# Kernel tuning notes

Hardware: AMD Instinct MI355X
Metric: run time of the kernel (lower is better)

## Reference

```python
import jax, jax.numpy as jnp
import numpy as np

E = 2048      # embed_dim
H = 16        # num_heads
HD = E // H // 2   # differential head dim = 64
S = 2048      # seq len
B = 1         # batch
DEPTH = 12
LAMBDA_INIT = 0.8 - 0.6 * float(np.exp(-0.3 * DEPTH))
EPS = 1e-5


def setup_inputs() -> dict:
    key = jax.random.key(0)
    ks = jax.random.split(key, 12)
    n = lambda k, shape, s=1.0: (jax.random.normal(k, shape, dtype=jnp.float32) * s)
    return {
        "query": n(ks[0], (S, B, E)),
        "key": n(ks[1], (S, B, E)),
        "value": n(ks[2], (S, B, E)),
        "rel_pos": 0,
        "attn_mask": jnp.zeros((B, S), dtype=jnp.bool_),
        "Wq": n(ks[3], (E, E), 0.02),
        "Wk": n(ks[4], (E, E), 0.02),
        "Wv": n(ks[5], (E, E), 0.02),
        "Wo": n(ks[6], (E, E), 0.02),
        "lq1": n(ks[7], (HD,), 0.1),
        "lk1": n(ks[8], (HD,), 0.1),
        "lq2": n(ks[9], (HD,), 0.1),
        "lk2": n(ks[10], (HD,), 0.1),
        "subln_g": jnp.ones((2 * HD,), dtype=jnp.float32),
    }


def reference(query, key, value, rel_pos, attn_mask,
              Wq, Wk, Wv, Wo, lq1, lk1, lq2, lk2, subln_g):
    # (S,B,E) -> (B,S,E)
    q = jnp.einsum("sbe,fe->bsf", query, Wq)
    k = jnp.einsum("sbe,fe->bsf", key, Wk)
    v = jnp.einsum("sbe,fe->bsf", value, Wv)

    bsz, tgt_len, _ = q.shape
    scaling = HD ** -0.5

    q = q.reshape(bsz, tgt_len, 2 * H, HD).transpose(0, 2, 1, 3) * scaling  # (B,2H,S,hd)
    k = k.reshape(bsz, tgt_len, 2 * H, HD).transpose(0, 2, 1, 3)            # (B,2H,S,hd)
    v = v.reshape(bsz, tgt_len, H, 2 * HD).transpose(0, 2, 1, 3)            # (B,H,S,2hd)

    scores = jnp.einsum("bhqd,bhkd->bhqk", q, k)  # (B,2H,S,S)
    mask = jnp.where(attn_mask[:, None, None, :], -jnp.inf, 0.0).astype(scores.dtype)
    scores = jnp.nan_to_num(scores + mask)  # torch.nan_to_num: nan->0, -inf->finite min

    probs = jax.nn.softmax(scores.astype(jnp.float32), axis=-1).astype(scores.dtype)
    probs = jnp.clip(probs, -1e6, 1e6)  # clamp as in original (dropout is identity in eval)

    lam1 = jnp.exp(jnp.sum(lq1 * lk1))
    lam2 = jnp.exp(jnp.sum(lq2 * lk2))
    lam_full = lam1 - lam2 + LAMBDA_INIT

    probs = probs.reshape(bsz, H, 2, tgt_len, tgt_len)
    diff = probs[:, :, 0] - lam_full * probs[:, :, 1]   # (B,H,S,S)

    attn = jnp.einsum("bhqk,bhkd->bhqd", diff, v)       # (B,H,S,2hd)

    # RMSNorm over last dim with affine weight
    rms = jax.lax.rsqrt(jnp.mean(jnp.square(attn), axis=-1, keepdims=True) + EPS)
    attn = attn * rms * subln_g
    attn = attn * (1.0 - LAMBDA_INIT)

    attn = attn.transpose(0, 2, 1, 3).reshape(bsz, tgt_len, H * 2 * HD)  # (B,S,E)
    attn = attn.transpose(1, 0, 2)                                       # (S,B,E)
    return jnp.einsum("sbe,fe->sbf", attn, Wo)
```

## Files before the change

### kernel.cpp

```cpp
#include <hip/hip_runtime.h>
#include <stdint.h>

#define LAMBDA_INIT_F 0.7836057665f

typedef __bf16 bf16x8 __attribute__((ext_vector_type(8)));
typedef float  f32x4  __attribute__((ext_vector_type(4)));
typedef unsigned short u16x8 __attribute__((ext_vector_type(8)));
typedef unsigned short u16x4 __attribute__((ext_vector_type(4)));
typedef short s16x4 __attribute__((ext_vector_type(4)));
typedef unsigned int u32x2 __attribute__((ext_vector_type(2)));
typedef unsigned int u32x4 __attribute__((ext_vector_type(4)));

__device__ __forceinline__ unsigned short f2b(float f) {
    union { float f; unsigned u; } v; v.f = f;
    unsigned u = v.u;
    return (unsigned short)((u + 0x7fffu + ((u >> 16) & 1u)) >> 16);
}

__device__ __forceinline__ unsigned pk2(float a, float b) {
    unsigned ua = __float_as_uint(a) + 0x8000u;
    unsigned ub = __float_as_uint(b) + 0x8000u;
    return __builtin_amdgcn_perm(ub, ua, 0x07060302u);
}

#if __has_builtin(__builtin_amdgcn_exp2f)
#define EXP2(x) __builtin_amdgcn_exp2f(x)
#else
__device__ __forceinline__ float EXP2(float x) {
    float r; asm volatile("v_exp_f32 %0, %1\n\ts_nop 1" : "=v"(r) : "v"(x)); return r;
}
#endif

#define GLD16(gp, sp) __builtin_amdgcn_global_load_lds( \
    (const __attribute__((address_space(1))) void*)(uintptr_t)(gp), \
    (__attribute__((address_space(3))) void*)(uint32_t)(uintptr_t)(sp), 16, 0, 0)

__global__ __launch_bounds__(256) void cvt7(const float* __restrict__ s0, const float* __restrict__ s1,
                                            const float* __restrict__ s2, const float* __restrict__ s3,
                                            const float* __restrict__ s4, const float* __restrict__ s5,
                                            const float* __restrict__ s6,
                                            unsigned short* __restrict__ dst) {
    int z = blockIdx.y;
    const float* s = z == 0 ? s0 : z == 1 ? s1 : z == 2 ? s2 : z == 3 ? s3 : z == 4 ? s4 : z == 5 ? s5 : s6;
    unsigned short* d = dst + (size_t)z * 4194304;
    size_t i = ((size_t)blockIdx.x * 256 + threadIdx.x) * 8;
    float4 a = *(const float4*)(s + i);
    float4 b = *(const float4*)(s + i + 4);
    u16x8 o;
    o[0] = f2b(a.x); o[1] = f2b(a.y); o[2] = f2b(a.z); o[3] = f2b(a.w);
    o[4] = f2b(b.x); o[5] = f2b(b.y); o[6] = f2b(b.z); o[7] = f2b(b.w);
    *(u16x8*)(d + i) = o;
}

template <int OUT_BF16, int NT, int DO_VT, int WPB>
__global__ __launch_bounds__(256, WPB) void gemm_bt(const unsigned short* __restrict__ Abase,
                                                    const unsigned short* __restrict__ Bbase,
                                                    void* __restrict__ Cbase,
                                                    unsigned short* __restrict__ VT,
                                                    float alpha0) {
    constexpr int MI = (NT == 128) ? 4 : 2;
    __shared__ __align__(16) unsigned short As[128 * 32];
    __shared__ __align__(16) unsigned short Bs[NT * 32];
    const int tid = threadIdx.x;
    const int w = tid >> 6, lane = tid & 63;
    const int quad = lane >> 4, l16 = lane & 15;
    const int b = blockIdx.z;
    const unsigned short* A = Abase + (size_t)b * 4194304;
    const unsigned short* B = Bbase + (size_t)b * 4194304;
    const float alpha = (b == 0) ? alpha0 : 1.0f;
    const int m0 = blockIdx.y * 128, n0 = blockIdx.x * NT;
    const int wm = (NT == 128) ? (w >> 1) * 64 : w * 32;
    const int wn = (NT == 128) ? (w & 1) * 64 : 0;
    const int sr = lane >> 2;
    const int sc = (((lane & 3) ^ ((lane >> 3) & 3)) * 8);
    const int rsw = ((l16 >> 1) & 3);

    f32x4 zz = {0.f, 0.f, 0.f, 0.f};
    f32x4 acc[MI][4];
#pragma unroll
    for (int i = 0; i < MI; ++i)
#pragma unroll
        for (int jn = 0; jn < 4; ++jn) acc[i][jn] = zz;

    for (int k0 = 0; k0 < 2048; k0 += 32) {
        GLD16(A + (size_t)(m0 + w * 16 + sr) * 2048 + k0 + sc,      &As[(w * 16) * 32]);
        GLD16(A + (size_t)(m0 + 64 + w * 16 + sr) * 2048 + k0 + sc, &As[(64 + w * 16) * 32]);
        if (NT == 128) {
            GLD16(B + (size_t)(n0 + w * 16 + sr) * 2048 + k0 + sc,      &Bs[(w * 16) * 32]);
            GLD16(B + (size_t)(n0 + 64 + w * 16 + sr) * 2048 + k0 + sc, &Bs[(64 + (w * 16)) * 32]);
        } else {
            GLD16(B + (size_t)(n0 + w * 16 + sr) * 2048 + k0 + sc, &Bs[(w * 16) * 32]);
        }
        __syncthreads();
        bf16x8 af[MI], bfr[4];
#pragma unroll
        for (int i = 0; i < MI; ++i) af[i]  = *(const bf16x8*)&As[(wm + i * 16 + l16) * 32 + (quad ^ rsw) * 8];
#pragma unroll
        for (int i = 0; i < 4; ++i)  bfr[i] = *(const bf16x8*)&Bs[(wn + i * 16 + l16) * 32 + (quad ^ rsw) * 8];
#pragma unroll
        for (int i = 0; i < MI; ++i)
#pragma unroll
            for (int jn = 0; jn < 4; ++jn)
                acc[i][jn] = __builtin_amdgcn_mfma_f32_16x16x32_bf16(af[i], bfr[jn], acc[i][jn], 0, 0, 0);
        __syncthreads();
    }

    if (DO_VT && b == 2) {
#pragma unroll
        for (int i = 0; i < MI; ++i)
#pragma unroll
            for (int jn = 0; jn < 4; ++jn) {
                int n = n0 + wn + jn * 16 + l16;
                int m = m0 + wm + i * 16 + quad * 4;
                u16x4 o;
#pragma unroll
                for (int r = 0; r < 4; ++r) o[r] = f2b(acc[i][jn][r]);
                *(u16x4*)&VT[(size_t)n * 2048 + m] = o;
            }
    } else {
#pragma unroll
        for (int i = 0; i < MI; ++i)
#pragma unroll
            for (int jn = 0; jn < 4; ++jn)
#pragma unroll
                for (int r = 0; r < 4; ++r) {
                    int row = m0 + wm + i * 16 + quad * 4 + r;
                    int col = n0 + wn + jn * 16 + l16;
                    float v = acc[i][jn][r] * alpha;
                    if (OUT_BF16)
                        ((unsigned short*)Cbase + (size_t)b * 4194304)[(size_t)row * 2048 + col] = f2b(v);
                    else
                        ((float*)Cbase)[(size_t)row * 2048 + col] = v;
                }
    }
}

__global__ __launch_bounds__(256, 2) void diff_attn(const unsigned short* __restrict__ qb,
                                                    const unsigned short* __restrict__ kb,
                                                    const unsigned short* __restrict__ vt,
                                                    const float* __restrict__ lq1,
                                                    const float* __restrict__ lk1,
                                                    const float* __restrict__ lq2,
                                                    const float* __restrict__ lk2,
                                                    const float* __restrict__ g,
                                                    unsigned short* __restrict__ Aout) {
    __shared__ __align__(16) unsigned short Ks[128 * 128];
    __shared__ __align__(16) unsigned short Vs[128 * 128];
    __shared__ float lam_s;
    const int tid = threadIdx.x, w = tid >> 6, lane = tid & 63;
    const int quad = lane >> 4, l16 = lane & 15;
    const int j = blockIdx.y;
    const int q0 = blockIdx.x * 64;

    if (tid < 64) {
        float p1 = lq1[tid] * lk1[tid];
        float p2 = lq2[tid] * lk2[tid];
        for (int off = 32; off; off >>= 1) { p1 += __shfl_xor(p1, off, 64); p2 += __shfl_xor(p2, off, 64); }
        if (tid == 0) lam_s = __expf(p1) - __expf(p2) + LAMBDA_INIT_F;
    }

    bf16x8 qf[2][2];
#pragma unroll
    for (int p = 0; p < 2; ++p)
#pragma unroll
        for (int dh = 0; dh < 2; ++dh)
            qf[p][dh] = *(const bf16x8*)&qb[(size_t)(q0 + w * 16 + l16) * 2048 + j * 128 + p * 64 + dh * 32 + quad * 8];

    f32x4 O[2][8];
#pragma unroll
    for (int p = 0; p < 2; ++p)
#pragma unroll
        for (int i = 0; i < 8; ++i)
#pragma unroll
            for (int r = 0; r < 4; ++r) O[p][i][r] = 0.f;
    float lsum[2] = {0.f, 0.f};

    const int srow = lane >> 4;

    for (int kv0 = 0; kv0 < 2048; kv0 += 128) {
#pragma unroll
        for (int t = 0; t < 8; ++t) {
            int rb = (w * 8 + t) * 4;
            int row = rb + srow;
            int cbs = (((lane & 15) ^ (row & 15)) * 8);
            GLD16(kb + (size_t)(kv0 + row) * 2048 + j * 128 + cbs, &Ks[rb * 128]);
            GLD16(vt + (size_t)(j * 128 + row) * 2048 + kv0 + cbs, &Vs[rb * 128]);
        }
        __syncthreads();

        u32x4 pd[2][4];
#pragma unroll
        for (int p = 0; p < 2; ++p) {
#pragma unroll
            for (int i = 0; i < 8; ++i) {
                bf16x8 a0 = *(const bf16x8*)&Ks[(i * 16 + l16) * 128 + ((p * 8 + quad) ^ l16) * 8];
                bf16x8 a1 = *(const bf16x8*)&Ks[(i * 16 + l16) * 128 + ((p * 8 + 4 + quad) ^ l16) * 8];
                f32x4 s = {0.f, 0.f, 0.f, 0.f};
                s = __builtin_amdgcn_mfma_f32_16x16x32_bf16(a0, qf[p][0], s, 0, 0, 0);
                s = __builtin_amdgcn_mfma_f32_16x16x32_bf16(a1, qf[p][1], s, 0, 0, 0);
                float e0 = EXP2(s[0]), e1 = EXP2(s[1]), e2 = EXP2(s[2]), e3 = EXP2(s[3]);
                lsum[p] += (e0 + e1) + (e2 + e3);
                pd[p][i >> 1][(i & 1) * 2]     = pk2(e0, e1);
                pd[p][i >> 1][(i & 1) * 2 + 1] = pk2(e2, e3);
            }
        }
#pragma unroll
        for (int u = 0; u < 4; ++u) {
            const int b0 = (4 * u + (quad >> 1)) ^ l16;
            const int b1 = (4 * u + 2 + (quad >> 1)) ^ l16;
#pragma unroll
            for (int dt = 0; dt < 8; ++dt) {
                const int rowoff = (dt * 16 + l16) * 128;
                u32x2 v0 = *(const u32x2*)&Vs[rowoff + b0 * 8 + (quad & 1) * 4];
                u32x2 v1 = *(const u32x2*)&Vs[rowoff + b1 * 8 + (quad & 1) * 4];
                u32x4 vv = {v0[0], v0[1], v1[0], v1[1]};
                bf16x8 vf8 = __builtin_bit_cast(bf16x8, vv);
                O[0][dt] = __builtin_amdgcn_mfma_f32_16x16x32_bf16(vf8, __builtin_bit_cast(bf16x8, pd[0][u]), O[0][dt], 0, 0, 0);
                O[1][dt] = __builtin_amdgcn_mfma_f32_16x16x32_bf16(vf8, __builtin_bit_cast(bf16x8, pd[1][u]), O[1][dt], 0, 0, 0);
            }
        }
        __syncthreads();
    }

#pragma unroll
    for (int p = 0; p < 2; ++p) {
        lsum[p] += __shfl_xor(lsum[p], 16, 64);
        lsum[p] += __shfl_xor(lsum[p], 32, 64);
    }
    const float inv1 = 1.0f / lsum[0];
    const float inv2 = lam_s / lsum[1];

    float ssum = 0.f;
#pragma unroll
    for (int dt = 0; dt < 8; ++dt)
#pragma unroll
        for (int r = 0; r < 4; ++r) {
            float v = O[0][dt][r] * inv1 - O[1][dt][r] * inv2;
            O[0][dt][r] = v;
            ssum += v * v;
        }
    ssum += __shfl_xor(ssum, 16, 64);
    ssum += __shfl_xor(ssum, 32, 64);
    const float rms = rsqrtf(ssum * (1.0f / 128.0f) + 1e-5f) * (1.0f - LAMBDA_INIT_F);

#pragma unroll
    for (int dt = 0; dt < 8; ++dt) {
        float4 g4 = *(const float4*)&g[dt * 16 + quad * 4];
        u16x4 o;
        o[0] = f2b(O[0][dt][0] * rms * g4.x);
        o[1] = f2b(O[0][dt][1] * rms * g4.y);
        o[2] = f2b(O[0][dt][2] * rms * g4.z);
        o[3] = f2b(O[0][dt][3] * rms * g4.w);
        *(u16x4*)&Aout[(size_t)(q0 + w * 16 + l16) * 2048 + j * 128 + dt * 16 + quad * 4] = o;
    }
}

extern "C" void kernel_launch(void* const* d_in, const int* in_sizes, int n_in,
                              void* d_out, int out_size, void* d_ws, size_t ws_size,
                              hipStream_t stream) {
    const float* query = (const float*)d_in[0];
    const float* key   = (const float*)d_in[1];
    const float* value = (const float*)d_in[2];
    const float* Wq  = (const float*)d_in[5];
    const float* Wk  = (const float*)d_in[6];
    const float* Wv  = (const float*)d_in[7];
    const float* Wo  = (const float*)d_in[8];
    const float* lq1 = (const float*)d_in[9];
    const float* lk1 = (const float*)d_in[10];
    const float* lq2 = (const float*)d_in[11];
    const float* lk2 = (const float*)d_in[12];
    const float* g   = (const float*)d_in[13];

    char* ws = (char*)d_ws;
    const size_t MB = 1ull << 20;
    const size_t N4 = 4194304;
    unsigned short* qb  = (unsigned short*)(ws + 0 * MB);
    unsigned short* vt  = (unsigned short*)(ws + 16 * MB);
    unsigned short* Aat = (unsigned short*)(ws + 24 * MB);
    unsigned short* Xq  = (unsigned short*)(ws + 32 * MB);
    float* lamp = (float*)(ws + 96 * MB);
    (void)lamp;

    const float alpha_q = 0.125f * 1.44269504f;

    cvt7<<<dim3(2048, 7), dim3(256), 0, stream>>>(query, key, value, Wq, Wk, Wv, Wo, Xq);
    gemm_bt<1, 128, 1, 3><<<dim3(16, 16, 3), dim3(256), 0, stream>>>(Xq, Xq + 3 * N4, (void*)qb, vt, alpha_q);
    diff_attn<<<dim3(32, 16), dim3(256), 0, stream>>>(qb, qb + N4, vt, lq1, lk1, lq2, lk2, g, Aat);
    gemm_bt<0, 64, 0, 2><<<dim3(32, 16, 1), dim3(256), 0, stream>>>(Aat, Xq + 6 * N4, d_out, nullptr, 1.0f);
}
```

Measured before the change: 331.8 us.

## Double-buffer K/V tiles in diff_attn and pre-permute V^T layout

The attention kernel moves from single-buffered 128-row K/V tiles to double-buffered 64-row tiles, prefetching the next tile with async global-to-LDS loads behind an explicit vmcnt wait, so loads overlap with MFMA compute. The V-transpose store in the projection GEMM now permutes columns so the attention kernel can read each V fragment with one 16-byte LDS load instead of two 8-byte loads. Blocks are also remapped on a 1D grid so that neighbouring blocks work on different heads, which changes how K/V data is shared in cache. The cost is more barriers per KV sweep, and correctness depends on the vmcnt count matching the number of loads issued per stage.

```diff
diff --git a/kernel.cpp b/kernel.cpp
--- a/kernel.cpp
+++ b/kernel.cpp
@@ -7,8 +7,6 @@
 typedef float  f32x4  __attribute__((ext_vector_type(4)));
 typedef unsigned short u16x8 __attribute__((ext_vector_type(8)));
 typedef unsigned short u16x4 __attribute__((ext_vector_type(4)));
-typedef short s16x4 __attribute__((ext_vector_type(4)));
-typedef unsigned int u32x2 __attribute__((ext_vector_type(2)));
 typedef unsigned int u32x4 __attribute__((ext_vector_type(4)));
 
 __device__ __forceinline__ unsigned short f2b(float f) {
@@ -112,10 +110,11 @@
             for (int jn = 0; jn < 4; ++jn) {
                 int n = n0 + wn + jn * 16 + l16;
                 int m = m0 + wm + i * 16 + quad * 4;
+                int sm = (m & ~31) | ((m & 12) << 1) | ((m & 16) >> 2) | (m & 3);
                 u16x4 o;
 #pragma unroll
                 for (int r = 0; r < 4; ++r) o[r] = f2b(acc[i][jn][r]);
-                *(u16x4*)&VT[(size_t)n * 2048 + m] = o;
+                *(u16x4*)&VT[(size_t)n * 2048 + sm] = o;
             }
     } else {
 #pragma unroll
@@ -144,13 +143,15 @@
                                                     const float* __restrict__ lk2,
                                                     const float* __restrict__ g,
                                                     unsigned short* __restrict__ Aout) {
-    __shared__ __align__(16) unsigned short Ks[128 * 128];
-    __shared__ __align__(16) unsigned short Vs[128 * 128];
+    __shared__ __align__(16) unsigned short Ks[2][64 * 128];
+    __shared__ __align__(16) unsigned short Vs[2][128 * 64];
     __shared__ float lam_s;
     const int tid = threadIdx.x, w = tid >> 6, lane = tid & 63;
     const int quad = lane >> 4, l16 = lane & 15;
-    const int j = blockIdx.y;
-    const int q0 = blockIdx.x * 64;
+    const int bid = blockIdx.x;
+    const int wrk = (bid & 7) * 64 + (bid >> 3);
+    const int j = wrk >> 5;
+    const int q0 = (wrk & 31) * 64;
 
     if (tid < 64) {
         float p1 = lq1[tid] * lk1[tid];
@@ -175,26 +176,42 @@
             for (int r = 0; r < 4; ++r) O[p][i][r] = 0.f;
     float lsum[2] = {0.f, 0.f};
 
-    const int srow = lane >> 4;
-
-    for (int kv0 = 0; kv0 < 2048; kv0 += 128) {
-#pragma unroll
-        for (int t = 0; t < 8; ++t) {
-            int rb = (w * 8 + t) * 4;
-            int row = rb + srow;
-            int cbs = (((lane & 15) ^ (row & 15)) * 8);
-            GLD16(kb + (size_t)(kv0 + row) * 2048 + j * 128 + cbs, &Ks[rb * 128]);
-            GLD16(vt + (size_t)(j * 128 + row) * 2048 + kv0 + cbs, &Vs[rb * 128]);
-        }
-        __syncthreads();
-
-        u32x4 pd[2][4];
+    const int srK = lane >> 4;
+    const int srV = lane >> 3;
+    const int scV = ((lane & 7) ^ (lane >> 3)) * 8;
+
+    auto STAGE = [&](int bsel, int kv0) {
+#pragma unroll
+        for (int t = 0; t < 4; ++t) {
+            int rowK = w * 16 + t * 4 + srK;
+            int cbsK = ((lane & 15) ^ (rowK & 15)) * 8;
+            GLD16(kb + (size_t)(kv0 + rowK) * 2048 + j * 128 + cbsK, &Ks[bsel][(w * 16 + t * 4) * 128]);
+        }
+#pragma unroll
+        for (int t = 0; t < 4; ++t) {
+            int rowV = w * 32 + t * 8 + srV;
+            GLD16(vt + (size_t)(j * 128 + rowV) * 2048 + kv0 + scV, &Vs[bsel][(w * 32 + t * 8) * 64]);
+        }
+    };
+
+    STAGE(0, 0);
+    for (int c = 0; c < 32; ++c) {
+        const int cur = c & 1;
+        if (c < 31) {
+            STAGE(cur ^ 1, (c + 1) * 64);
+            asm volatile("s_waitcnt vmcnt(8)" ::: "memory");
+        } else {
+            asm volatile("s_waitcnt vmcnt(0)" ::: "memory");
+        }
+        __builtin_amdgcn_s_barrier();
+
+        u32x4 pd[2][2];
 #pragma unroll
         for (int p = 0; p < 2; ++p) {
 #pragma unroll
-            for (int i = 0; i < 8; ++i) {
-                bf16x8 a0 = *(const bf16x8*)&Ks[(i * 16 + l16) * 128 + ((p * 8 + quad) ^ l16) * 8];
-                bf16x8 a1 = *(const bf16x8*)&Ks[(i * 16 + l16) * 128 + ((p * 8 + 4 + quad) ^ l16) * 8];
+            for (int i = 0; i < 4; ++i) {
+                bf16x8 a0 = *(const bf16x8*)&Ks[cur][(i * 16 + l16) * 128 + ((p * 8 + quad) ^ l16) * 8];
+                bf16x8 a1 = *(const bf16x8*)&Ks[cur][(i * 16 + l16) * 128 + ((p * 8 + 4 + quad) ^ l16) * 8];
                 f32x4 s = {0.f, 0.f, 0.f, 0.f};
                 s = __builtin_amdgcn_mfma_f32_16x16x32_bf16(a0, qf[p][0], s, 0, 0, 0);
                 s = __builtin_amdgcn_mfma_f32_16x16x32_bf16(a1, qf[p][1], s, 0, 0, 0);
@@ -205,21 +222,16 @@
             }
         }
 #pragma unroll
-        for (int u = 0; u < 4; ++u) {
-            const int b0 = (4 * u + (quad >> 1)) ^ l16;
-            const int b1 = (4 * u + 2 + (quad >> 1)) ^ l16;
+        for (int u = 0; u < 2; ++u) {
+            const int blk = (((4 * u + quad) ^ (l16 & 7))) * 8;
 #pragma unroll
             for (int dt = 0; dt < 8; ++dt) {
-                const int rowoff = (dt * 16 + l16) * 128;
-                u32x2 v0 = *(const u32x2*)&Vs[rowoff + b0 * 8 + (quad & 1) * 4];
-                u32x2 v1 = *(const u32x2*)&Vs[rowoff + b1 * 8 + (quad & 1) * 4];
-                u32x4 vv = {v0[0], v0[1], v1[0], v1[1]};
-                bf16x8 vf8 = __builtin_bit_cast(bf16x8, vv);
+                bf16x8 vf8 = *(const bf16x8*)&Vs[cur][(dt * 16 + l16) * 64 + blk];
                 O[0][dt] = __builtin_amdgcn_mfma_f32_16x16x32_bf16(vf8, __builtin_bit_cast(bf16x8, pd[0][u]), O[0][dt], 0, 0, 0);
                 O[1][dt] = __builtin_amdgcn_mfma_f32_16x16x32_bf16(vf8, __builtin_bit_cast(bf16x8, pd[1][u]), O[1][dt], 0, 0, 0);
             }
         }
-        __syncthreads();
+        __builtin_amdgcn_s_barrier();
     }
 
 #pragma unroll
@@ -278,13 +290,11 @@
     unsigned short* vt  = (unsigned short*)(ws + 16 * MB);
     unsigned short* Aat = (unsigned short*)(ws + 24 * MB);
     unsigned short* Xq  = (unsigned short*)(ws + 32 * MB);
-    float* lamp = (float*)(ws + 96 * MB);
-    (void)lamp;
 
     const float alpha_q = 0.125f * 1.44269504f;
 
     cvt7<<<dim3(2048, 7), dim3(256), 0, stream>>>(query, key, value, Wq, Wk, Wv, Wo, Xq);
     gemm_bt<1, 128, 1, 3><<<dim3(16, 16, 3), dim3(256), 0, stream>>>(Xq, Xq + 3 * N4, (void*)qb, vt, alpha_q);
-    diff_attn<<<dim3(32, 16), dim3(256), 0, stream>>>(qb, qb + N4, vt, lq1, lk1, lq2, lk2, g, Aat);
+    diff_attn<<<dim3(512), dim3(256), 0, stream>>>(qb, qb + N4, vt, lq1, lk1, lq2, lk2, g, Aat);
     gemm_bt<0, 64, 0, 2><<<dim3(32, 16, 1), dim3(256), 0, stream>>>(Aat, Xq + 6 * N4, d_out, nullptr, 1.0f);
 }
```

New measurement: 312.2 us. -5.9%, faster.
